# Kernel tuning notes

Hardware: AMD Instinct MI355X
Metric: run time of the kernel (lower is better)

## Reference

```python
import jax, jax.numpy as jnp
import numpy as np

N_NODES = 100000
N_EDGES = 1200000
D_IN = 16
D_EDGE = 4
H = 64


def setup_inputs() -> dict:
    key = jax.random.key(0)
    ks = jax.random.split(key, 20)
    s = 0.05
    inp = {
        "src": jax.random.randint(ks[0], (N_EDGES,), 0, N_NODES),
        "dst": jax.random.randint(ks[1], (N_EDGES,), 0, N_NODES),
        "t": jax.random.uniform(ks[2], (N_EDGES,), dtype=jnp.float32),
        "x": jax.random.normal(ks[3], (N_NODES, D_IN), dtype=jnp.float32),
        "edge_attr": jax.random.normal(ks[4], (N_EDGES, D_EDGE), dtype=jnp.float32),
        # x_encoder
        "Wx": jax.random.normal(ks[5], (D_IN, H), dtype=jnp.float32) * s,
        "bx": jnp.zeros((H,), dtype=jnp.float32),
        # TransformerConv (heads=1, concat=False)
        "Wq": jax.random.normal(ks[6], (H, H), dtype=jnp.float32) * s,
        "bq": jnp.zeros((H,), dtype=jnp.float32),
        "Wk": jax.random.normal(ks[7], (H, H), dtype=jnp.float32) * s,
        "bk": jnp.zeros((H,), dtype=jnp.float32),
        "Wv": jax.random.normal(ks[8], (H, H), dtype=jnp.float32) * s,
        "bv": jnp.zeros((H,), dtype=jnp.float32),
        "We": jax.random.normal(ks[9], (D_EDGE, H), dtype=jnp.float32) * s,  # lin_edge, bias=False
        "Ws": jax.random.normal(ks[10], (H, H), dtype=jnp.float32) * s,  # lin_skip (root weight)
        "bs": jnp.zeros((H,), dtype=jnp.float32),
        # MLP head
        "W1": jax.random.normal(ks[11], (H, 8), dtype=jnp.float32) * s,
        "b1": jnp.zeros((8,), dtype=jnp.float32),
        "W2": jax.random.normal(ks[12], (8, 1), dtype=jnp.float32) * s,
        "b2": jnp.zeros((1,), dtype=jnp.float32),
    }
    return inp


def reference(src, dst, t, x, edge_attr, Wx, bx, Wq, bq, Wk, bk, Wv, bv, We, Ws, bs, W1, b1, W2, b2):
    # eval mode: dropouts are identity; TGN memory.update_state is a pure
    # side effect and does not influence the returned output.
    xe = x @ Wx + bx                             # [N, H]

    # TransformerConv, heads=1, concat=False, flow src -> dst
    q = xe @ Wq + bq                             # [N, H]
    k = xe @ Wk + bk                             # [N, H]
    v = xe @ Wv + bv                             # [N, H]
    e = edge_attr @ We                           # [E, H]

    k_e = k[src] + e                             # [E, H]
    v_e = v[src] + e                             # [E, H]
    alpha = jnp.sum(q[dst] * k_e, axis=-1) / jnp.sqrt(jnp.float32(H))  # [E]

    # softmax over incoming edges per destination node
    m = jax.ops.segment_max(alpha, dst, num_segments=N_NODES)
    a = jnp.exp(alpha - m[dst])
    denom = jax.ops.segment_sum(a, dst, num_segments=N_NODES)
    w = a / (denom[dst] + 1e-16)                 # [E]

    agg = jax.ops.segment_sum(v_e * w[:, None], dst, num_segments=N_NODES)  # [N, H]
    h_local = agg + (xe @ Ws + bs)               # root/skip connection

    h = h_local[dst]                             # [E, H]
    h = jax.nn.relu(h @ W1 + b1)                 # [E, 8]
    out = (h @ W2 + b2)[:, 0]                    # [E]
    return out
```

## Files before the change

kernel.cpp:

```cpp
#include <hip/hip_runtime.h>

#define OFF_M   0
#define OFF_U   256
#define OFF_W   272
#define OFF_C   288
#define OFF_R   292
#define OFF_R0  356
#define OFF_PV  360
#define OFF_PE  488
#define OFF_PS  520
#define OFF_BH1 648
#define OFF_BH2 656
#define CST_N   664

#define NB      64
#define CAPB    1152
#define CHE     4096
#define MAXBUCK 2048

typedef int nint4 __attribute__((ext_vector_type(4)));

__device__ __forceinline__ unsigned f2bf(float f) {
    unsigned u = __float_as_uint(f);
    u += 0x7fffu + ((u >> 16) & 1u);
    return u >> 16;
}
__device__ __forceinline__ float bf_lo(unsigned u) { return __uint_as_float(u << 16); }
__device__ __forceinline__ float bf_hi(unsigned u) { return __uint_as_float(u & 0xffff0000u); }

struct Params {
    const int* src; const int* dst; const float4* ea4; const float* x;
    const float* Wx; const float* bx;
    const float* Wq; const float* bq;
    const float* Wk; const float* bk;
    const float* Wv; const float* bv;
    const float* We; const float* Ws; const float* bs;
    const float* W1; const float* b1; const float* W2; const float* b2;
    float* cst;
    float* srec;
    float* drec;
    float* xps;
    float* g;
    nint4* recs;
    int* gcur;
    float* out;
    int N, E;
};

__device__ void do_fold(const Params& P, float* __restrict__ cst)
{
    __shared__ float sWf[4][16][64];
    __shared__ float sbf[4][64];
    const int t = threadIdx.x;
    const int c = t & 63, m = t >> 6;
    const float* W; const float* b;
    switch (m) {
        case 0:  W = P.Wq; b = P.bq; break;
        case 1:  W = P.Wk; b = P.bk; break;
        case 2:  W = P.Wv; b = P.bv; break;
        default: W = P.Ws; b = P.bs; break;
    }
    float acc[16];
#pragma unroll
    for (int i = 0; i < 16; ++i) acc[i] = 0.f;
    float bacc = b[c];
    for (int j = 0; j < 64; ++j) {
        const float wv = W[j * 64 + c];
        bacc += P.bx[j] * wv;
#pragma unroll
        for (int i = 0; i < 16; ++i) acc[i] += P.Wx[i * 64 + j] * wv;
    }
#pragma unroll
    for (int i = 0; i < 16; ++i) sWf[m][i][c] = acc[i];
    sbf[m][c] = bacc;
    __syncthreads();

    {
        const int i = t >> 4, j = t & 15;
        float s = 0.f;
        for (int cc = 0; cc < 64; ++cc) s += sWf[0][i][cc] * sWf[1][j][cc];
        cst[OFF_M + i * 16 + j] = s;
    }
    if (t < 16) {
        float su = 0.f, sw = 0.f;
        for (int cc = 0; cc < 64; ++cc) {
            su += sWf[1][t][cc] * sbf[0][cc];
            sw += sWf[0][t][cc] * sbf[1][cc];
        }
        cst[OFF_U + t] = su;
        cst[OFF_W + t] = sw;
    }
    if (t == 0) {
        float s = 0.f;
        for (int cc = 0; cc < 64; ++cc) s += sbf[0][cc] * sbf[1][cc];
        cst[OFF_C] = s;
    }
    if (t < 64) {
        const int j = t >> 4, i = t & 15;
        float s = 0.f;
        for (int cc = 0; cc < 64; ++cc) s += P.We[j * 64 + cc] * sWf[0][i][cc];
        cst[OFF_R + j * 16 + i] = s;
    }
    if (t < 4) {
        float s = 0.f;
        for (int cc = 0; cc < 64; ++cc) s += P.We[t * 64 + cc] * sbf[0][cc];
        cst[OFF_R0 + t] = s;
    }
    if (t < 128) {
        const int i = t >> 3, j = t & 7;
        float sv = 0.f, ss = 0.f;
        for (int cc = 0; cc < 64; ++cc) {
            const float w1 = P.W1[cc * 8 + j];
            sv += sWf[2][i][cc] * w1;
            ss += sWf[3][i][cc] * w1;
        }
        cst[OFF_PV + i * 8 + j] = sv;
        cst[OFF_PS + i * 8 + j] = ss;
    }
    if (t < 32) {
        const int mm = t >> 3, j = t & 7;
        float s = 0.f;
        for (int cc = 0; cc < 64; ++cc) s += P.We[mm * 64 + cc] * P.W1[cc * 8 + j];
        cst[OFF_PE + mm * 8 + j] = s;
    }
    if (t < 8) {
        float s1 = 0.f, s2 = 0.f;
        for (int cc = 0; cc < 64; ++cc) {
            const float w1 = P.W1[cc * 8 + t];
            s1 += sbf[2][cc] * w1;
            s2 += sbf[3][cc] * w1;
        }
        cst[OFF_BH1 + t] = s1;
        cst[OFF_BH2 + t] = s2 + P.b1[t];
    }
}

__global__ __launch_bounds__(256) void k_init(Params P)
{
    if (blockIdx.x == 0) { do_fold(P, P.cst); return; }
    const int nbuck = (P.N + NB - 1) >> 6;
    const int i = ((int)blockIdx.x - 1) * 256 + threadIdx.x;
    if (i < nbuck) P.gcur[i] = 0;
}

__global__ __launch_bounds__(256) void k_node(Params P)
{
    __shared__ float sx[16][16];
    const float* __restrict__ cst = P.cst;
    const int t = threadIdx.x;
    const int node0 = blockIdx.x * 16;
    const int nl = t >> 4, cg = t & 15;
    {
        const int idx = node0 * 16 + t;
        sx[nl][cg] = (idx < P.N * 16) ? P.x[idx] : 0.f;
    }
    __syncthreads();
    const int n = node0 + nl;
    if (n >= P.N) return;

    float y = cst[OFF_U + cg];
#pragma unroll
    for (int i = 0; i < 16; ++i)
        y += sx[nl][i] * cst[OFF_M + i * 16 + cg];

    const float xv = sx[nl][cg];
    const float yp = __shfl_xor(y, 1);
    const float xp = __shfl_xor(xv, 1);
    if ((cg & 1) == 0) {
        ((unsigned*)P.drec)[(size_t)n * 16 + (cg >> 1)] = f2bf(y) | (f2bf(yp) << 16);
        ((unsigned*)P.srec)[(size_t)n * 16 + (cg >> 1)] = f2bf(xv) | (f2bf(xp) << 16);
    }

    if (cg < 8) {
        float s = 0.f;
#pragma unroll
        for (int i = 0; i < 16; ++i)
            s += sx[nl][i] * cst[OFF_PV + i * 8 + cg];
        P.srec[(size_t)n * 16 + 8 + cg] = s;
    } else {
        const int j = cg - 8;
        float s = 0.f;
#pragma unroll
        for (int i = 0; i < 16; ++i)
            s += sx[nl][i] * cst[OFF_PS + i * 8 + j];
        P.xps[(size_t)n * 8 + j] = s;
    }
    if (cg < 4) {
        float r = cst[OFF_R0 + cg];
#pragma unroll
        for (int i = 0; i < 16; ++i)
            r += cst[OFF_R + cg * 16 + i] * sx[nl][i];
        P.drec[(size_t)n * 16 + 8 + cg] = r;
    }
}

__global__ __launch_bounds__(256) void k_bin(Params P)
{
    __shared__ int lh[MAXBUCK];
    const int t = threadIdx.x;
    const int nbuck = (P.N + NB - 1) >> 6;
    for (int b = t; b < nbuck; b += 256) lh[b] = 0;
    __syncthreads();

    const int e0 = blockIdx.x * CHE;
    const int eend = min(e0 + CHE, P.E);
    for (int e = e0 + t; e < eend; e += 256)
        atomicAdd(&lh[P.dst[e] >> 6], 1);
    __syncthreads();

    for (int b = t; b < nbuck; b += 256) {
        const int c = lh[b];
        lh[b] = c ? atomicAdd(&P.gcur[b], c) : 0;
    }
    __syncthreads();

    for (int e = e0 + t; e < eend; e += 256) {
        const int d = P.dst[e];
        const int b = d >> 6;
        const int pos = atomicAdd(&lh[b], 1);
        if (pos < CAPB) {
            const float4 A = P.ea4[e];
            nint4 r;
            r.x = P.src[e];
            r.y = d & (NB - 1);
            r.z = (int)(f2bf(A.x) | (f2bf(A.y) << 16));
            r.w = (int)(f2bf(A.z) | (f2bf(A.w) << 16));
            P.recs[(size_t)b * CAPB + pos] = r;
        }
    }
}

__global__ __launch_bounds__(256) void k_agg(Params P)
{
    __shared__ unsigned sdy[NB * 8];
    __shared__ float sdrv[NB * 4];
    __shared__ float sacc[NB * 10];
    const int t = threadIdx.x;
    const int b = blockIdx.x;
    const int n0 = b << 6;
    const float* __restrict__ cst = P.cst;

    const unsigned* dr = (const unsigned*)P.drec + (size_t)n0 * 16;
    for (int i = t; i < NB * 16; i += 256) {
        const int m = i >> 4, j = i & 15;
        const unsigned w = dr[i];
        if (j < 8) sdy[m * 8 + j] = w;
        else if (j < 12) sdrv[m * 4 + (j - 8)] = __uint_as_float(w);
    }
    for (int i = t; i < NB * 10; i += 256) sacc[i] = 0.f;
    __syncthreads();

    const int cnt = min(P.gcur[b], CAPB);
    const int G = t >> 3;
    const int cg = t & 7;
    const float pe0 = cst[OFF_PE + 0 * 8 + cg];
    const float pe1 = cst[OFF_PE + 1 * 8 + cg];
    const float pe2 = cst[OFF_PE + 2 * 8 + cg];
    const float pe3 = cst[OFF_PE + 3 * 8 + cg];
    const nint4* __restrict__ rb = P.recs + (size_t)b * CAPB;

    for (int i = G; i < cnt; i += 32) {
        const nint4 r = rb[i];
        const int s = r.x, dl = r.y;
        const float A0 = bf_lo((unsigned)r.z), A1 = bf_hi((unsigned)r.z);
        const float A2 = bf_lo((unsigned)r.w), A3 = bf_hi((unsigned)r.w);
        const unsigned xw = ((const unsigned*)P.srec)[(size_t)s * 16 + cg];
        const float pvs = P.srec[(size_t)s * 16 + 8 + cg];
        const unsigned yw = sdy[dl * 8 + cg];

        float p = bf_lo(xw) * bf_lo(yw) + bf_hi(xw) * bf_hi(yw);
        p += __shfl_xor(p, 1);
        p += __shfl_xor(p, 2);
        p += __shfl_xor(p, 4);
        p += A0 * sdrv[dl * 4 + 0] + A1 * sdrv[dl * 4 + 1]
           + A2 * sdrv[dl * 4 + 2] + A3 * sdrv[dl * 4 + 3];
        const float a = __expf(p * 0.125f);

        atomicAdd(&sacc[dl * 10 + cg], a * (pvs + A0 * pe0 + A1 * pe1 + A2 * pe2 + A3 * pe3));
        if (cg == 0) atomicAdd(&sacc[dl * 10 + 8], a);
    }
    __syncthreads();

    if (t < NB) {
        const int n = n0 + t;
        if (n < P.N) {
            const float den = sacc[t * 10 + 8];
            const float inv = 1.f / (den + 1e-16f);
            const float dinv = den * inv;
            float val = P.b2[0];
#pragma unroll
            for (int j = 0; j < 8; ++j) {
                const float hid = inv * sacc[t * 10 + j]
                                + P.xps[(size_t)n * 8 + j]
                                + dinv * cst[OFF_BH1 + j] + cst[OFF_BH2 + j];
                val += fmaxf(hid, 0.f) * P.W2[j];
            }
            P.g[n] = val;
        }
    }
}

__global__ __launch_bounds__(256) void k_out(
    const int* __restrict__ dst, const float* __restrict__ g,
    float* __restrict__ out, int E)
{
    const int e = blockIdx.x * 256 + threadIdx.x;
    if (e < E) out[e] = g[dst[e]];
}

extern "C" void kernel_launch(void* const* d_in, const int* in_sizes, int n_in,
                              void* d_out, int out_size, void* d_ws, size_t ws_size,
                              hipStream_t stream)
{
    Params P;
    P.src = (const int*)d_in[0];
    P.dst = (const int*)d_in[1];
    P.x   = (const float*)d_in[3];
    P.ea4 = (const float4*)d_in[4];
    P.Wx  = (const float*)d_in[5];
    P.bx  = (const float*)d_in[6];
    P.Wq  = (const float*)d_in[7];
    P.bq  = (const float*)d_in[8];
    P.Wk  = (const float*)d_in[9];
    P.bk  = (const float*)d_in[10];
    P.Wv  = (const float*)d_in[11];
    P.bv  = (const float*)d_in[12];
    P.We  = (const float*)d_in[13];
    P.Ws  = (const float*)d_in[14];
    P.bs  = (const float*)d_in[15];
    P.W1  = (const float*)d_in[16];
    P.b1  = (const float*)d_in[17];
    P.W2  = (const float*)d_in[18];
    P.b2  = (const float*)d_in[19];

    P.E = in_sizes[0];
    P.N = in_sizes[3] / 16;
    P.out = (float*)d_out;

    const int nbuck = (P.N + NB - 1) >> 6;

    float* w = (float*)d_ws;
    P.recs = (nint4*)w;   w += (size_t)nbuck * CAPB * 4;
    P.srec = w;           w += (size_t)P.N * 16;
    P.drec = w;           w += (size_t)P.N * 16;
    P.xps  = w;           w += (size_t)P.N * 8;
    P.g    = w;           w += (size_t)P.N;
    P.gcur = (int*)w;     w += nbuck;
    P.cst  = w;

    const int nbE = (P.E + 255) / 256;

    k_init<<<1 + (nbuck + 255) / 256, 256, 0, stream>>>(P);
    k_node<<<(P.N + 15) / 16, 256, 0, stream>>>(P);
    k_bin<<<(P.E + CHE - 1) / CHE, 256, 0, stream>>>(P);
    k_agg<<<nbuck, 256, 0, stream>>>(P);
    k_out<<<nbE, 256, 0, stream>>>(P.dst, P.g, P.out, P.E);
}
```

Before: 270.7 us.

## Software-pipeline edge gathers in k_agg and register-cache dst in larger k_bin blocks

The aggregation loop now prefetches the record two iterations ahead and the source-node gather one iteration ahead, so the dependent global loads overlap with the current edge's compute and shared-memory atomics. The binning kernel uses 512-thread blocks over 8192-edge chunks and keeps each thread's 16 dst indices in registers, so dst is read from memory once instead of twice. The fold loops get partial unroll pragmas. The cost is more registers per thread and fewer binning blocks, roughly 147 instead of 293, which may lower occupancy and parallelism on a 256-CU device.

```diff
diff --git a/kernel.cpp b/kernel.cpp
--- a/kernel.cpp
+++ b/kernel.cpp
@@ -15,7 +15,7 @@
 
 #define NB      64
 #define CAPB    1152
-#define CHE     4096
+#define CHB     8192
 #define MAXBUCK 2048
 
 typedef int nint4 __attribute__((ext_vector_type(4)));
@@ -64,6 +64,7 @@
 #pragma unroll
     for (int i = 0; i < 16; ++i) acc[i] = 0.f;
     float bacc = b[c];
+#pragma unroll 8
     for (int j = 0; j < 64; ++j) {
         const float wv = W[j * 64 + c];
         bacc += P.bx[j] * wv;
@@ -78,11 +79,13 @@
     {
         const int i = t >> 4, j = t & 15;
         float s = 0.f;
+#pragma unroll 8
         for (int cc = 0; cc < 64; ++cc) s += sWf[0][i][cc] * sWf[1][j][cc];
         cst[OFF_M + i * 16 + j] = s;
     }
     if (t < 16) {
         float su = 0.f, sw = 0.f;
+#pragma unroll 8
         for (int cc = 0; cc < 64; ++cc) {
             su += sWf[1][t][cc] * sbf[0][cc];
             sw += sWf[0][t][cc] * sbf[1][cc];
@@ -92,23 +95,27 @@
     }
     if (t == 0) {
         float s = 0.f;
+#pragma unroll 8
         for (int cc = 0; cc < 64; ++cc) s += sbf[0][cc] * sbf[1][cc];
         cst[OFF_C] = s;
     }
     if (t < 64) {
         const int j = t >> 4, i = t & 15;
         float s = 0.f;
+#pragma unroll 8
         for (int cc = 0; cc < 64; ++cc) s += P.We[j * 64 + cc] * sWf[0][i][cc];
         cst[OFF_R + j * 16 + i] = s;
     }
     if (t < 4) {
         float s = 0.f;
+#pragma unroll 8
         for (int cc = 0; cc < 64; ++cc) s += P.We[t * 64 + cc] * sbf[0][cc];
         cst[OFF_R0 + t] = s;
     }
     if (t < 128) {
         const int i = t >> 3, j = t & 7;
         float sv = 0.f, ss = 0.f;
+#pragma unroll 8
         for (int cc = 0; cc < 64; ++cc) {
             const float w1 = P.W1[cc * 8 + j];
             sv += sWf[2][i][cc] * w1;
@@ -120,11 +127,13 @@
     if (t < 32) {
         const int mm = t >> 3, j = t & 7;
         float s = 0.f;
+#pragma unroll 8
         for (int cc = 0; cc < 64; ++cc) s += P.We[mm * 64 + cc] * P.W1[cc * 8 + j];
         cst[OFF_PE + mm * 8 + j] = s;
     }
     if (t < 8) {
         float s1 = 0.f, s2 = 0.f;
+#pragma unroll 8
         for (int cc = 0; cc < 64; ++cc) {
             const float w1 = P.W1[cc * 8 + t];
             s1 += sbf[2][cc] * w1;
@@ -194,30 +203,40 @@
     }
 }
 
-__global__ __launch_bounds__(256) void k_bin(Params P)
+__global__ __launch_bounds__(512) void k_bin(Params P)
 {
     __shared__ int lh[MAXBUCK];
     const int t = threadIdx.x;
     const int nbuck = (P.N + NB - 1) >> 6;
-    for (int b = t; b < nbuck; b += 256) lh[b] = 0;
-    __syncthreads();
-
-    const int e0 = blockIdx.x * CHE;
-    const int eend = min(e0 + CHE, P.E);
-    for (int e = e0 + t; e < eend; e += 256)
-        atomicAdd(&lh[P.dst[e] >> 6], 1);
-    __syncthreads();
-
-    for (int b = t; b < nbuck; b += 256) {
+    for (int b = t; b < nbuck; b += 512) lh[b] = 0;
+    __syncthreads();
+
+    const int e0 = blockIdx.x * CHB;
+    const int nval = min(CHB, P.E - e0);
+    int dreg[16];
+#pragma unroll
+    for (int k = 0; k < 16; ++k) {
+        const int o = t + k * 512;
+        dreg[k] = (o < nval) ? P.dst[e0 + o] : -1;
+    }
+#pragma unroll
+    for (int k = 0; k < 16; ++k)
+        if (dreg[k] >= 0) atomicAdd(&lh[dreg[k] >> 6], 1);
+    __syncthreads();
+
+    for (int b = t; b < nbuck; b += 512) {
         const int c = lh[b];
         lh[b] = c ? atomicAdd(&P.gcur[b], c) : 0;
     }
     __syncthreads();
 
-    for (int e = e0 + t; e < eend; e += 256) {
-        const int d = P.dst[e];
-        const int b = d >> 6;
-        const int pos = atomicAdd(&lh[b], 1);
+#pragma unroll
+    for (int k = 0; k < 16; ++k) {
+        const int d = dreg[k];
+        if (d < 0) continue;
+        const int e = e0 + t + k * 512;
+        const int bb = d >> 6;
+        const int pos = atomicAdd(&lh[bb], 1);
         if (pos < CAPB) {
             const float4 A = P.ea4[e];
             nint4 r;
@@ -225,7 +244,7 @@
             r.y = d & (NB - 1);
             r.z = (int)(f2bf(A.x) | (f2bf(A.y) << 16));
             r.w = (int)(f2bf(A.z) | (f2bf(A.w) << 16));
-            P.recs[(size_t)b * CAPB + pos] = r;
+            P.recs[(size_t)bb * CAPB + pos] = r;
         }
     }
 }
@@ -258,26 +277,40 @@
     const float pe2 = cst[OFF_PE + 2 * 8 + cg];
     const float pe3 = cst[OFF_PE + 3 * 8 + cg];
     const nint4* __restrict__ rb = P.recs + (size_t)b * CAPB;
-
-    for (int i = G; i < cnt; i += 32) {
-        const nint4 r = rb[i];
-        const int s = r.x, dl = r.y;
-        const float A0 = bf_lo((unsigned)r.z), A1 = bf_hi((unsigned)r.z);
-        const float A2 = bf_lo((unsigned)r.w), A3 = bf_hi((unsigned)r.w);
-        const unsigned xw = ((const unsigned*)P.srec)[(size_t)s * 16 + cg];
-        const float pvs = P.srec[(size_t)s * 16 + 8 + cg];
-        const unsigned yw = sdy[dl * 8 + cg];
-
-        float p = bf_lo(xw) * bf_lo(yw) + bf_hi(xw) * bf_hi(yw);
-        p += __shfl_xor(p, 1);
-        p += __shfl_xor(p, 2);
-        p += __shfl_xor(p, 4);
-        p += A0 * sdrv[dl * 4 + 0] + A1 * sdrv[dl * 4 + 1]
-           + A2 * sdrv[dl * 4 + 2] + A3 * sdrv[dl * 4 + 3];
-        const float a = __expf(p * 0.125f);
-
-        atomicAdd(&sacc[dl * 10 + cg], a * (pvs + A0 * pe0 + A1 * pe1 + A2 * pe2 + A3 * pe3));
-        if (cg == 0) atomicAdd(&sacc[dl * 10 + 8], a);
+    const unsigned* __restrict__ sr = (const unsigned*)P.srec;
+
+    if (G < cnt) {
+        const int iB0 = G + 32;
+        nint4 rA = rb[G];
+        nint4 rB = rb[iB0 < cnt ? iB0 : G];
+        unsigned xwA = sr[(size_t)rA.x * 16 + cg];
+        float pvsA = __uint_as_float(sr[(size_t)rA.x * 16 + 8 + cg]);
+
+        for (int i = G; i < cnt; i += 32) {
+            const int iC = i + 64;
+            const nint4 rC = rb[iC < cnt ? iC : i];
+            const unsigned xwB = sr[(size_t)rB.x * 16 + cg];
+            const float pvsB = __uint_as_float(sr[(size_t)rB.x * 16 + 8 + cg]);
+
+            const int dl = rA.y;
+            const float A0 = bf_lo((unsigned)rA.z), A1 = bf_hi((unsigned)rA.z);
+            const float A2 = bf_lo((unsigned)rA.w), A3 = bf_hi((unsigned)rA.w);
+            const unsigned yw = sdy[dl * 8 + cg];
+
+            float p = bf_lo(xwA) * bf_lo(yw) + bf_hi(xwA) * bf_hi(yw);
+            p += __shfl_xor(p, 1);
+            p += __shfl_xor(p, 2);
+            p += __shfl_xor(p, 4);
+            p += A0 * sdrv[dl * 4 + 0] + A1 * sdrv[dl * 4 + 1]
+               + A2 * sdrv[dl * 4 + 2] + A3 * sdrv[dl * 4 + 3];
+            const float a = __expf(p * 0.125f);
+
+            atomicAdd(&sacc[dl * 10 + cg],
+                      a * (pvsA + A0 * pe0 + A1 * pe1 + A2 * pe2 + A3 * pe3));
+            if (cg == 0) atomicAdd(&sacc[dl * 10 + 8], a);
+
+            rA = rB; rB = rC; xwA = xwB; pvsA = pvsB;
+        }
     }
     __syncthreads();
 
@@ -352,7 +385,7 @@
 
     k_init<<<1 + (nbuck + 255) / 256, 256, 0, stream>>>(P);
     k_node<<<(P.N + 15) / 16, 256, 0, stream>>>(P);
-    k_bin<<<(P.E + CHE - 1) / CHE, 256, 0, stream>>>(P);
+    k_bin<<<(P.E + CHB - 1) / CHB, 512, 0, stream>>>(P);
     k_agg<<<nbuck, 256, 0, stream>>>(P);
     k_out<<<nbE, 256, 0, stream>>>(P.dst, P.g, P.out, P.E);
 }
```

Result: faster. 257.0 us (-5.0%).
